# Kernel optimization log

Measured on AMD Instinct MI355X. Metric: run time of the kernel, lower is better.

The kernel has to match this reference:

```python
import jax, jax.numpy as jnp
import numpy as np

N = 100000      # nodes
E = 1250000     # edges
IN = 128        # in_channels
H = 64          # hidden_channels
L = 2           # num_layers (GCNConv count)
EPS = 1e-5      # BatchNorm eps


def setup_inputs() -> dict:
    key = jax.random.key(0)
    ks = jax.random.split(key, 10)
    x = jax.random.normal(ks[0], (N, IN), jnp.float32)
    edge_index = jax.random.randint(ks[1], (2, E), 0, N, dtype=jnp.int32)
    fc_w = jax.random.normal(ks[2], (IN, H), jnp.float32) / np.sqrt(IN)
    fc_b = jax.random.normal(ks[3], (H,), jnp.float32) * 0.01
    conv_w = jax.random.normal(ks[4], (L, H, H), jnp.float32) / np.sqrt(H)
    conv_b = jax.random.normal(ks[5], (L, H), jnp.float32) * 0.01
    bn_gamma = jnp.ones((L + 1, H), jnp.float32)
    bn_beta = jnp.zeros((L + 1, H), jnp.float32)
    bn_mean = jax.random.normal(ks[6], (L + 1, H), jnp.float32) * 0.1
    bn_var = jax.random.uniform(ks[7], (L + 1, H), jnp.float32) + 0.5
    return {"x": x, "edge_index": edge_index, "fc_w": fc_w, "fc_b": fc_b,
            "conv_w": conv_w, "conv_b": conv_b, "bn_gamma": bn_gamma,
            "bn_beta": bn_beta, "bn_mean": bn_mean, "bn_var": bn_var}


def reference(x, edge_index, fc_w, fc_b, conv_w, conv_b, bn_gamma, bn_beta, bn_mean, bn_var):
    n = x.shape[0]
    loops = jnp.arange(n, dtype=edge_index.dtype)
    src = jnp.concatenate([edge_index[0], loops])   # add self-loops (GCNConv default)
    dst = jnp.concatenate([edge_index[1], loops])
    # symmetric normalization: deg computed on destination, norm = d_s^-1/2 * d_d^-1/2
    deg = jax.ops.segment_sum(jnp.ones_like(dst, x.dtype), dst, num_segments=n)
    dis = jax.lax.rsqrt(deg)                        # deg >= 1 thanks to self-loops
    norm = dis[src] * dis[dst]                      # [E+N]

    def bn(h, i):  # eval-mode BatchNorm1d with running stats
        return (h - bn_mean[i]) * (bn_gamma[i] * jax.lax.rsqrt(bn_var[i] + EPS)) + bn_beta[i]

    h = jax.nn.relu(bn(x @ fc_w + fc_b, 0))         # [N, H]; dropout is identity in eval
    last = h
    for i in range(conv_w.shape[0]):
        hw = h @ conv_w[i]                          # GCNConv: transform then aggregate
        agg = jax.ops.segment_sum(hw[src] * norm[:, None], dst, num_segments=n) + conv_b[i]
        h = jax.nn.relu(bn(agg, i + 1)) + last      # residual to post-fc activation
    return h
```

## Files before the change

kernel.cpp:

```cpp
#include <hip/hip_runtime.h>

#define NNODES 100000
#define NEDGES 1250000
#define IN_CH 128
#define HID 64
#define BN_EPS 1e-5f

#define NPAD 100352
#define BIN_N 256
#define BINW 391
#define BIN_CHUNK 2048
#define BIN_BLOCKS 611
#define BIN_CAP_LDS 16
#define BIN_REGION 10000
#define MM_BLOCKS 1563
#define GBLOCKS 3125
#define ELL_C 32
#define OVF_CAP 65536

typedef __attribute__((ext_vector_type(8))) short s16x8;
typedef __attribute__((ext_vector_type(4))) float f32x4;

__device__ __forceinline__ ushort f2bf(float f) {
    union { float f; unsigned int i; } c;
    c.f = f;
    unsigned int lsb = (c.i >> 16) & 1u;
    return (ushort)((c.i + 0x7FFFu + lsb) >> 16);
}
__device__ __forceinline__ float asf(unsigned int i) {
    union { unsigned int i; float f; } c;
    c.i = i;
    return c.f;
}

__device__ __forceinline__ void ell_insert(int d, int soff, int* slot,
                                           int* ell, int* ovf_n, int2* ovf) {
    int s = atomicAdd(&slot[d], 1);
    if (s < ELL_C) ell[(d << 5) + s] = soff;
    else {
        int oi = atomicAdd(ovf_n, 1);
        if (oi < OVF_CAP) ovf[oi] = make_int2(d, soff);
    }
}

__device__ __forceinline__ void fc_body(
        int blk, int tid,
        const float* __restrict__ x, const float* __restrict__ w,
        const float* __restrict__ bb,
        const float* __restrict__ g, const float* __restrict__ be,
        const float* __restrict__ mu, const float* __restrict__ var,
        ushort* __restrict__ h0) {
    const int wave = tid >> 6;
    const int lane = tid & 63;
    const int m = lane & 15;
    const int q = lane >> 4;
    const int node_base = (blk * 4 + wave) * 16;

    s16x8 bfrag[4][4];
#pragma unroll
    for (int kc = 0; kc < 4; ++kc)
#pragma unroll
        for (int ct = 0; ct < 4; ++ct)
#pragma unroll
            for (int j = 0; j < 8; ++j)
                bfrag[kc][ct][j] = (short)f2bf(w[(kc * 32 + q * 8 + j) * HID + ct * 16 + m]);

    f32x4 acc[4] = {{0,0,0,0},{0,0,0,0},{0,0,0,0},{0,0,0,0}};

    int row = node_base + m;
    if (row >= NNODES) row = NNODES - 1;
    const float4* xp = (const float4*)(x + (size_t)row * IN_CH + q * 8);

#pragma unroll
    for (int kc = 0; kc < 4; ++kc) {
        float4 a0 = xp[kc * 8 + 0];
        float4 a1 = xp[kc * 8 + 1];
        s16x8 af;
        af[0] = (short)f2bf(a0.x); af[1] = (short)f2bf(a0.y);
        af[2] = (short)f2bf(a0.z); af[3] = (short)f2bf(a0.w);
        af[4] = (short)f2bf(a1.x); af[5] = (short)f2bf(a1.y);
        af[6] = (short)f2bf(a1.z); af[7] = (short)f2bf(a1.w);
#pragma unroll
        for (int ct = 0; ct < 4; ++ct)
            acc[ct] = __builtin_amdgcn_mfma_f32_16x16x32_bf16(af, bfrag[kc][ct], acc[ct], 0, 0, 0);
    }

#pragma unroll
    for (int ct = 0; ct < 4; ++ct) {
        int col = ct * 16 + m;
        float sc = g[col] * rsqrtf(var[col] + BN_EPS);
        float off = (bb[col] - mu[col]) * sc + be[col];
#pragma unroll
        for (int r = 0; r < 4; ++r) {
            int node = node_base + q * 4 + r;
            if (node < NNODES)
                h0[(size_t)node * HID + col] =
                    f2bf(fmaxf(acc[ct][r] * sc + off, 0.f));
        }
    }
}

__global__ __launch_bounds__(256) void bin_fc(
        const int* __restrict__ src, const int* __restrict__ dst,
        unsigned int* __restrict__ staged, int* bin_n,
        int* slot, int* __restrict__ ell, int* ovf_n, int2* __restrict__ ovf,
        const float* __restrict__ x, const float* __restrict__ w,
        const float* __restrict__ bb,
        const float* __restrict__ g, const float* __restrict__ be,
        const float* __restrict__ mu, const float* __restrict__ var,
        ushort* __restrict__ h0) {
    __shared__ unsigned int sbin[BIN_N][BIN_CAP_LDS];
    __shared__ int scnt[BIN_N];
    __shared__ int sbase[BIN_N];
    const int tid = threadIdx.x;

    if (blockIdx.x >= BIN_BLOCKS) {
        fc_body(blockIdx.x - BIN_BLOCKS, tid, x, w, bb, g, be, mu, var, h0);
        return;
    }

    scnt[tid] = 0;
    __syncthreads();

    const int base = blockIdx.x * (BIN_CHUNK / 4);
    const int4* dst4 = (const int4*)dst;
    const int4* src4 = (const int4*)src;
#pragma unroll
    for (int k = 0; k < BIN_CHUNK / 1024; ++k) {
        int i = base + k * 256 + tid;
        if (i < NEDGES / 4) {
            int4 dv = dst4[i];
            int4 sv = src4[i];
#define BIN_ONE(D, S)                                                       \
            {                                                               \
                int b_ = (D) / BINW;                                        \
                unsigned int pk_ = ((unsigned int)((D) - b_ * BINW) << 17)  \
                                   | (unsigned int)(S);                     \
                int sl_ = atomicAdd(&scnt[b_], 1);                          \
                if (sl_ < BIN_CAP_LDS) sbin[b_][sl_] = pk_;                 \
                else ell_insert((D), (S) << 7, slot, ell, ovf_n, ovf);      \
            }
            BIN_ONE(dv.x, sv.x)
            BIN_ONE(dv.y, sv.y)
            BIN_ONE(dv.z, sv.z)
            BIN_ONE(dv.w, sv.w)
#undef BIN_ONE
        }
    }
    __syncthreads();
    {
        int c = scnt[tid];
        if (c > BIN_CAP_LDS) c = BIN_CAP_LDS;
        sbase[tid] = atomicAdd(&bin_n[tid], c);
    }
    __syncthreads();
    const int wave = tid >> 6;
    const int lane = tid & 63;
    for (int grp = wave; grp < BIN_N / 4; grp += 4) {
        int b = grp * 4 + (lane >> 4);
        int s = lane & 15;
        int c = scnt[b];
        if (c > BIN_CAP_LDS) c = BIN_CAP_LDS;
        if (s < c) {
            int gidx = sbase[b] + s;
            unsigned int v = sbin[b][s];
            if (gidx < BIN_REGION) {
                staged[(size_t)b * BIN_REGION + gidx] = v;
            } else {
                int d = b * BINW + (int)(v >> 17);
                ell_insert(d, (int)(v & 0x1FFFFu) << 7, slot, ell, ovf_n, ovf);
            }
        }
    }
}

__global__ __launch_bounds__(1024) void ell_fill(
        const unsigned int* __restrict__ staged, const int* __restrict__ bin_n,
        int* slot, int* __restrict__ ell, int* ovf_n, int2* __restrict__ ovf) {
    const int b = blockIdx.x;
    int n = bin_n[b];
    if (n > BIN_REGION) n = BIN_REGION;
    const unsigned int* sp = staged + (size_t)b * BIN_REGION;
    const int lo = b * BINW;
    int i = threadIdx.x;
    for (; i + 3072 < n; i += 4096) {
        unsigned int v0 = sp[i];
        unsigned int v1 = sp[i + 1024];
        unsigned int v2 = sp[i + 2048];
        unsigned int v3 = sp[i + 3072];
        ell_insert(lo + (int)(v0 >> 17), (int)(v0 & 0x1FFFFu) << 7, slot, ell, ovf_n, ovf);
        ell_insert(lo + (int)(v1 >> 17), (int)(v1 & 0x1FFFFu) << 7, slot, ell, ovf_n, ovf);
        ell_insert(lo + (int)(v2 >> 17), (int)(v2 & 0x1FFFFu) << 7, slot, ell, ovf_n, ovf);
        ell_insert(lo + (int)(v3 >> 17), (int)(v3 & 0x1FFFFu) << 7, slot, ell, ovf_n, ovf);
    }
    for (; i < n; i += 1024) {
        unsigned int v = sp[i];
        ell_insert(lo + (int)(v >> 17), (int)(v & 0x1FFFFu) << 7, slot, ell, ovf_n, ovf);
    }
}

__global__ __launch_bounds__(256) void conv_mm_l1(
        const ushort* __restrict__ h, const float* __restrict__ w,
        const int* __restrict__ deg, ushort* __restrict__ hws) {
    const int tid = threadIdx.x;
    const int wave = tid >> 6;
    const int lane = tid & 63;
    const int m = lane & 15;
    const int q = lane >> 4;
    const int node_base = (blockIdx.x * 4 + wave) * 16;

    s16x8 bfrag[2][4];
#pragma unroll
    for (int kc = 0; kc < 2; ++kc)
#pragma unroll
        for (int ct = 0; ct < 4; ++ct)
#pragma unroll
            for (int j = 0; j < 8; ++j)
                bfrag[kc][ct][j] = (short)f2bf(w[(kc * 32 + q * 8 + j) * HID + ct * 16 + m]);

    f32x4 acc[4] = {{0,0,0,0},{0,0,0,0},{0,0,0,0},{0,0,0,0}};

    int row = node_base + m;
    if (row >= NNODES) row = NNODES - 1;

#pragma unroll
    for (int kc = 0; kc < 2; ++kc) {
        const s16x8* hp = (const s16x8*)(h + (size_t)row * HID + kc * 32 + q * 8);
        s16x8 af = *hp;
#pragma unroll
        for (int ct = 0; ct < 4; ++ct)
            acc[ct] = __builtin_amdgcn_mfma_f32_16x16x32_bf16(af, bfrag[kc][ct], acc[ct], 0, 0, 0);
    }

    float dv[4];
#pragma unroll
    for (int r = 0; r < 4; ++r) {
        int node = node_base + q * 4 + r;
        dv[r] = (node < NNODES) ? rsqrtf((float)(deg[node] + 1)) : 0.f;
    }
#pragma unroll
    for (int ct = 0; ct < 4; ++ct) {
#pragma unroll
        for (int r = 0; r < 4; ++r) {
            int node = node_base + q * 4 + r;
            if (node < NNODES)
                hws[(size_t)node * HID + ct * 16 + m] = f2bf(acc[ct][r] * dv[r]);
        }
    }
}

__global__ __launch_bounds__(256) void gather_conv(
        const ushort* __restrict__ hws,
        const int* __restrict__ deg, const int* __restrict__ ell,
        const int* __restrict__ ovf_n, const int2* __restrict__ ovf,
        const float* __restrict__ bias,
        const float* __restrict__ g, const float* __restrict__ be,
        const float* __restrict__ mu, const float* __restrict__ var,
        const ushort* __restrict__ last,
        const float* __restrict__ w2,
        ushort* __restrict__ hws2) {
    __shared__ ushort sh[32][72];
    const int wave = threadIdx.x >> 6;
    const int lane = threadIdx.x & 63;
    const int grp  = lane >> 3;
    const int j    = lane & 7;
    const int d = blockIdx.x * 32 + wave * 8 + grp;
    const unsigned int moff = (unsigned int)j * 16u;
    const unsigned int doff = ((unsigned int)d << 7) + moff;

    const char* hb = (const char*)hws;

    uint4 lv = *(const uint4*)((const char*)last + doff);

    float a[8];
    {
        uint4 sv = *(const uint4*)(hb + doff);
        a[0] = asf(sv.x << 16); a[1] = asf(sv.x & 0xffff0000u);
        a[2] = asf(sv.y << 16); a[3] = asf(sv.y & 0xffff0000u);
        a[4] = asf(sv.z << 16); a[5] = asf(sv.z & 0xffff0000u);
        a[6] = asf(sv.w << 16); a[7] = asf(sv.w & 0xffff0000u);
    }

#define ACC8(V)                                                         \
    a[0] += asf((V).x << 16); a[1] += asf((V).x & 0xffff0000u);         \
    a[2] += asf((V).y << 16); a[3] += asf((V).y & 0xffff0000u);         \
    a[4] += asf((V).z << 16); a[5] += asf((V).z & 0xffff0000u);         \
    a[6] += asf((V).w << 16); a[7] += asf((V).w & 0xffff0000u);

    const int n = deg[d];
    const int nn = (n < ELL_C) ? n : ELL_C;
    const int* sp = ell + ((size_t)d << 5);

    int k = 0;
    for (; k + 8 <= nn; k += 8) {
        unsigned int o0 = (unsigned int)sp[k + 0] + moff;
        unsigned int o1 = (unsigned int)sp[k + 1] + moff;
        unsigned int o2 = (unsigned int)sp[k + 2] + moff;
        unsigned int o3 = (unsigned int)sp[k + 3] + moff;
        unsigned int o4 = (unsigned int)sp[k + 4] + moff;
        unsigned int o5 = (unsigned int)sp[k + 5] + moff;
        unsigned int o6 = (unsigned int)sp[k + 6] + moff;
        unsigned int o7 = (unsigned int)sp[k + 7] + moff;
        uint4 v0 = *(const uint4*)(hb + o0);
        uint4 v1 = *(const uint4*)(hb + o1);
        uint4 v2 = *(const uint4*)(hb + o2);
        uint4 v3 = *(const uint4*)(hb + o3);
        uint4 v4 = *(const uint4*)(hb + o4);
        uint4 v5 = *(const uint4*)(hb + o5);
        uint4 v6 = *(const uint4*)(hb + o6);
        uint4 v7 = *(const uint4*)(hb + o7);
        ACC8(v0) ACC8(v1) ACC8(v2) ACC8(v3)
        ACC8(v4) ACC8(v5) ACC8(v6) ACC8(v7)
    }
    for (; k + 4 <= nn; k += 4) {
        unsigned int o0 = (unsigned int)sp[k + 0] + moff;
        unsigned int o1 = (unsigned int)sp[k + 1] + moff;
        unsigned int o2 = (unsigned int)sp[k + 2] + moff;
        unsigned int o3 = (unsigned int)sp[k + 3] + moff;
        uint4 v0 = *(const uint4*)(hb + o0);
        uint4 v1 = *(const uint4*)(hb + o1);
        uint4 v2 = *(const uint4*)(hb + o2);
        uint4 v3 = *(const uint4*)(hb + o3);
        ACC8(v0) ACC8(v1) ACC8(v2) ACC8(v3)
    }
    for (; k < nn; ++k) {
        uint4 v = *(const uint4*)(hb + ((unsigned int)sp[k] + moff));
        ACC8(v)
    }
    if (n > ELL_C) {
        int on = *ovf_n;
        if (on > OVF_CAP) on = OVF_CAP;
        for (int jj = 0; jj < on; ++jj) {
            int2 e = ovf[jj];
            if (e.x == d) {
                uint4 v = *(const uint4*)(hb + ((unsigned int)e.y + moff));
                ACC8(v)
            }
        }
    }
#undef ACC8

    float dd = rsqrtf((float)(n + 1));
    float4 bi0 = ((const float4*)bias)[2 * j], bi1 = ((const float4*)bias)[2 * j + 1];
    float4 g0  = ((const float4*)g)[2 * j],    g1  = ((const float4*)g)[2 * j + 1];
    float4 be0 = ((const float4*)be)[2 * j],   be1 = ((const float4*)be)[2 * j + 1];
    float4 mu0 = ((const float4*)mu)[2 * j],   mu1 = ((const float4*)mu)[2 * j + 1];
    float4 va0 = ((const float4*)var)[2 * j],  va1 = ((const float4*)var)[2 * j + 1];
    float l0 = asf(lv.x << 16), l1 = asf(lv.x & 0xffff0000u);
    float l2 = asf(lv.y << 16), l3 = asf(lv.y & 0xffff0000u);
    float l4 = asf(lv.z << 16), l5 = asf(lv.z & 0xffff0000u);
    float l6 = asf(lv.w << 16), l7 = asf(lv.w & 0xffff0000u);

#define EPI(A, BI, GV, BE, MU, VA, LO) \
    (fmaxf(((A) * dd + (BI) - (MU)) * ((GV) * rsqrtf((VA) + BN_EPS)) + (BE), 0.f) + (LO))
    float r0 = EPI(a[0], bi0.x, g0.x, be0.x, mu0.x, va0.x, l0);
    float r1 = EPI(a[1], bi0.y, g0.y, be0.y, mu0.y, va0.y, l1);
    float r2 = EPI(a[2], bi0.z, g0.z, be0.z, mu0.z, va0.z, l2);
    float r3 = EPI(a[3], bi0.w, g0.w, be0.w, mu0.w, va0.w, l3);
    float r4 = EPI(a[4], bi1.x, g1.x, be1.x, mu1.x, va1.x, l4);
    float r5 = EPI(a[5], bi1.y, g1.y, be1.y, mu1.y, va1.y, l5);
    float r6 = EPI(a[6], bi1.z, g1.z, be1.z, mu1.z, va1.z, l6);
    float r7 = EPI(a[7], bi1.w, g1.w, be1.w, mu1.w, va1.w, l7);
#undef EPI

    {
        const int rloc = wave * 8 + grp;
        uint4 o;
        o.x = (unsigned int)f2bf(r0 * dd) | ((unsigned int)f2bf(r1 * dd) << 16);
        o.y = (unsigned int)f2bf(r2 * dd) | ((unsigned int)f2bf(r3 * dd) << 16);
        o.z = (unsigned int)f2bf(r4 * dd) | ((unsigned int)f2bf(r5 * dd) << 16);
        o.w = (unsigned int)f2bf(r6 * dd) | ((unsigned int)f2bf(r7 * dd) << 16);
        *(uint4*)(&sh[rloc][j * 8]) = o;
    }
    __syncthreads();

    {
        const int rt = wave >> 1;
        const int cbase = (wave & 1) * 2;
        const int m = lane & 15;
        const int q = lane >> 4;

        s16x8 bfrag[2][2];
#pragma unroll
        for (int kc = 0; kc < 2; ++kc)
#pragma unroll
            for (int c = 0; c < 2; ++c)
#pragma unroll
                for (int jj = 0; jj < 8; ++jj)
                    bfrag[kc][c][jj] = (short)f2bf(
                        w2[(kc * 32 + q * 8 + jj) * HID + (cbase + c) * 16 + m]);

        f32x4 acc2[2] = {{0,0,0,0},{0,0,0,0}};
#pragma unroll
        for (int kc = 0; kc < 2; ++kc) {
            s16x8 af = *(const s16x8*)(&sh[rt * 16 + m][kc * 32 + q * 8]);
#pragma unroll
            for (int c = 0; c < 2; ++c)
                acc2[c] = __builtin_amdgcn_mfma_f32_16x16x32_bf16(
                    af, bfrag[kc][c], acc2[c], 0, 0, 0);
        }

        const int node_base = blockIdx.x * 32 + rt * 16;
#pragma unroll
        for (int c = 0; c < 2; ++c) {
            const int col = (cbase + c) * 16 + m;
#pragma unroll
            for (int r = 0; r < 4; ++r) {
                int node = node_base + q * 4 + r;
                hws2[(size_t)node * HID + col] = f2bf(acc2[c][r]);
            }
        }
    }
}

__global__ __launch_bounds__(256) void gather_update(
        const ushort* __restrict__ hws,
        const int* __restrict__ deg, const int* __restrict__ ell,
        const int* __restrict__ ovf_n, const int2* __restrict__ ovf,
        const float* __restrict__ bias,
        const float* __restrict__ g, const float* __restrict__ be,
        const float* __restrict__ mu, const float* __restrict__ var,
        const ushort* __restrict__ last,
        float* __restrict__ out_f) {
    const int wave = threadIdx.x >> 6;
    const int lane = threadIdx.x & 63;
    const int grp  = lane >> 3;
    const int j    = lane & 7;
    const int d = blockIdx.x * 32 + wave * 8 + grp;
    const unsigned int moff = (unsigned int)j * 16u;
    const unsigned int doff = ((unsigned int)d << 7) + moff;

    const char* hb = (const char*)hws;

    uint4 lv = *(const uint4*)((const char*)last + doff);

    float a[8];
    {
        uint4 sv = *(const uint4*)(hb + doff);
        a[0] = asf(sv.x << 16); a[1] = asf(sv.x & 0xffff0000u);
        a[2] = asf(sv.y << 16); a[3] = asf(sv.y & 0xffff0000u);
        a[4] = asf(sv.z << 16); a[5] = asf(sv.z & 0xffff0000u);
        a[6] = asf(sv.w << 16); a[7] = asf(sv.w & 0xffff0000u);
    }

#define ACC8(V)                                                         \
    a[0] += asf((V).x << 16); a[1] += asf((V).x & 0xffff0000u);         \
    a[2] += asf((V).y << 16); a[3] += asf((V).y & 0xffff0000u);         \
    a[4] += asf((V).z << 16); a[5] += asf((V).z & 0xffff0000u);         \
    a[6] += asf((V).w << 16); a[7] += asf((V).w & 0xffff0000u);

    const int n = deg[d];
    const int nn = (n < ELL_C) ? n : ELL_C;
    const int* sp = ell + ((size_t)d << 5);

    int k = 0;
    for (; k + 8 <= nn; k += 8) {
        unsigned int o0 = (unsigned int)sp[k + 0] + moff;
        unsigned int o1 = (unsigned int)sp[k + 1] + moff;
        unsigned int o2 = (unsigned int)sp[k + 2] + moff;
        unsigned int o3 = (unsigned int)sp[k + 3] + moff;
        unsigned int o4 = (unsigned int)sp[k + 4] + moff;
        unsigned int o5 = (unsigned int)sp[k + 5] + moff;
        unsigned int o6 = (unsigned int)sp[k + 6] + moff;
        unsigned int o7 = (unsigned int)sp[k + 7] + moff;
        uint4 v0 = *(const uint4*)(hb + o0);
        uint4 v1 = *(const uint4*)(hb + o1);
        uint4 v2 = *(const uint4*)(hb + o2);
        uint4 v3 = *(const uint4*)(hb + o3);
        uint4 v4 = *(const uint4*)(hb + o4);
        uint4 v5 = *(const uint4*)(hb + o5);
        uint4 v6 = *(const uint4*)(hb + o6);
        uint4 v7 = *(const uint4*)(hb + o7);
        ACC8(v0) ACC8(v1) ACC8(v2) ACC8(v3)
        ACC8(v4) ACC8(v5) ACC8(v6) ACC8(v7)
    }
    for (; k + 4 <= nn; k += 4) {
        unsigned int o0 = (unsigned int)sp[k + 0] + moff;
        unsigned int o1 = (unsigned int)sp[k + 1] + moff;
        unsigned int o2 = (unsigned int)sp[k + 2] + moff;
        unsigned int o3 = (unsigned int)sp[k + 3] + moff;
        uint4 v0 = *(const uint4*)(hb + o0);
        uint4 v1 = *(const uint4*)(hb + o1);
        uint4 v2 = *(const uint4*)(hb + o2);
        uint4 v3 = *(const uint4*)(hb + o3);
        ACC8(v0) ACC8(v1) ACC8(v2) ACC8(v3)
    }
    for (; k < nn; ++k) {
        uint4 v = *(const uint4*)(hb + ((unsigned int)sp[k] + moff));
        ACC8(v)
    }
    if (n > ELL_C) {
        int on = *ovf_n;
        if (on > OVF_CAP) on = OVF_CAP;
        for (int jj = 0; jj < on; ++jj) {
            int2 e = ovf[jj];
            if (e.x == d) {
                uint4 v = *(const uint4*)(hb + ((unsigned int)e.y + moff));
                ACC8(v)
            }
        }
    }
#undef ACC8

    float dd = rsqrtf((float)(n + 1));
    float4 bi0 = ((const float4*)bias)[2 * j], bi1 = ((const float4*)bias)[2 * j + 1];
    float4 g0  = ((const float4*)g)[2 * j],    g1  = ((const float4*)g)[2 * j + 1];
    float4 be0 = ((const float4*)be)[2 * j],   be1 = ((const float4*)be)[2 * j + 1];
    float4 mu0 = ((const float4*)mu)[2 * j],   mu1 = ((const float4*)mu)[2 * j + 1];
    float4 va0 = ((const float4*)var)[2 * j],  va1 = ((const float4*)var)[2 * j + 1];
    float l0 = asf(lv.x << 16), l1 = asf(lv.x & 0xffff0000u);
    float l2 = asf(lv.y << 16), l3 = asf(lv.y & 0xffff0000u);
    float l4 = asf(lv.z << 16), l5 = asf(lv.z & 0xffff0000u);
    float l6 = asf(lv.w << 16), l7 = asf(lv.w & 0xffff0000u);

#define EPI(A, BI, GV, BE, MU, VA, LO) \
    (fmaxf(((A) * dd + (BI) - (MU)) * ((GV) * rsqrtf((VA) + BN_EPS)) + (BE), 0.f) + (LO))
    float r0 = EPI(a[0], bi0.x, g0.x, be0.x, mu0.x, va0.x, l0);
    float r1 = EPI(a[1], bi0.y, g0.y, be0.y, mu0.y, va0.y, l1);
    float r2 = EPI(a[2], bi0.z, g0.z, be0.z, mu0.z, va0.z, l2);
    float r3 = EPI(a[3], bi0.w, g0.w, be0.w, mu0.w, va0.w, l3);
    float r4 = EPI(a[4], bi1.x, g1.x, be1.x, mu1.x, va1.x, l4);
    float r5 = EPI(a[5], bi1.y, g1.y, be1.y, mu1.y, va1.y, l5);
    float r6 = EPI(a[6], bi1.z, g1.z, be1.z, mu1.z, va1.z, l6);
    float r7 = EPI(a[7], bi1.w, g1.w, be1.w, mu1.w, va1.w, l7);
#undef EPI

    float4* op = (float4*)(out_f + (size_t)d * HID + j * 8);
    op[0] = make_float4(r0, r1, r2, r3);
    op[1] = make_float4(r4, r5, r6, r7);
}

extern "C" void kernel_launch(void* const* d_in, const int* in_sizes, int n_in,
                              void* d_out, int out_size, void* d_ws, size_t ws_size,
                              hipStream_t stream) {
    const float* x      = (const float*)d_in[0];
    const int*   eidx   = (const int*)d_in[1];
    const float* fc_w   = (const float*)d_in[2];
    const float* fc_b   = (const float*)d_in[3];
    const float* conv_w = (const float*)d_in[4];
    const float* conv_b = (const float*)d_in[5];
    const float* bn_g   = (const float*)d_in[6];
    const float* bn_b   = (const float*)d_in[7];
    const float* bn_m   = (const float*)d_in[8];
    const float* bn_v   = (const float*)d_in[9];

    const int* src = eidx;
    const int* dst = eidx + NEDGES;
    float* out = (float*)d_out;

    int*    slot    = (int*)d_ws;
    int*    meta    = slot + NPAD;
    int*    ovf_n   = meta;
    int*    bin_n   = meta + 16;
    int2*   ovf     = (int2*)(meta + 272);
    int*    ell     = (int*)(ovf + OVF_CAP);
    ushort* h0      = (ushort*)(ell + (size_t)NNODES * ELL_C);
    ushort* hws2    = h0 + (size_t)NNODES * HID;
    ushort* hws     = hws2 + (size_t)NNODES * HID;
    unsigned int* staged = (unsigned int*)(hws + (size_t)NNODES * HID);

    const int BLK = 256;

    hipMemsetAsync(slot, 0, (size_t)(NPAD + 272) * 4, stream);

    bin_fc<<<BIN_BLOCKS + MM_BLOCKS, BLK, 0, stream>>>(
        src, dst, staged, bin_n, slot, ell, ovf_n, ovf,
        x, fc_w, fc_b, bn_g, bn_b, bn_m, bn_v, h0);

    ell_fill<<<BIN_N, 1024, 0, stream>>>(staged, bin_n, slot, ell, ovf_n, ovf);

    conv_mm_l1<<<MM_BLOCKS, BLK, 0, stream>>>(h0, conv_w, slot, hws);

    gather_conv<<<GBLOCKS, BLK, 0, stream>>>(hws, slot, ell, ovf_n, ovf,
                                             conv_b, bn_g + HID, bn_b + HID,
                                             bn_m + HID, bn_v + HID, h0,
                                             conv_w + HID * HID, hws2);

    gather_update<<<GBLOCKS, BLK, 0, stream>>>(hws2, slot, ell, ovf_n, ovf,
                                               conv_b + HID, bn_g + 2 * HID, bn_b + 2 * HID,
                                               bn_m + 2 * HID, bn_v + 2 * HID,
                                               h0, out);
}
```

Measured before the change: 271.3 us.

## Fuse ELL fill with layer-1 matmul using block-local LDS slot counters

The ELL fill now runs per destination bin with slot counters kept in shared memory instead of global atomics, then writes the counts to global slot. The layer-1 transform matmul is fused into the same kernel, using the LDS degree counts for the normalisation, which removes one launch and the large slot memset. Edges that overflowed LDS during binning go to a first overflow list that every fill block scans, adding redundant reads in exchange for avoiding global atomics. The overflow capacity is reduced, and each bin's matmul over 391 nodes runs in two passes of 16-row tiles per wave.

```diff
diff --git a/kernel.cpp b/kernel.cpp
--- a/kernel.cpp
+++ b/kernel.cpp
@@ -16,7 +16,7 @@
 #define MM_BLOCKS 1563
 #define GBLOCKS 3125
 #define ELL_C 32
-#define OVF_CAP 65536
+#define OVF_CAP 16384
 
 typedef __attribute__((ext_vector_type(8))) short s16x8;
 typedef __attribute__((ext_vector_type(4))) float f32x4;
@@ -31,16 +31,6 @@
     union { unsigned int i; float f; } c;
     c.i = i;
     return c.f;
-}
-
-__device__ __forceinline__ void ell_insert(int d, int soff, int* slot,
-                                           int* ell, int* ovf_n, int2* ovf) {
-    int s = atomicAdd(&slot[d], 1);
-    if (s < ELL_C) ell[(d << 5) + s] = soff;
-    else {
-        int oi = atomicAdd(ovf_n, 1);
-        if (oi < OVF_CAP) ovf[oi] = make_int2(d, soff);
-    }
 }
 
 __device__ __forceinline__ void fc_body(
@@ -103,7 +93,7 @@
 __global__ __launch_bounds__(256) void bin_fc(
         const int* __restrict__ src, const int* __restrict__ dst,
         unsigned int* __restrict__ staged, int* bin_n,
-        int* slot, int* __restrict__ ell, int* ovf_n, int2* __restrict__ ovf,
+        int* ovf1_n, int2* __restrict__ ovf1,
         const float* __restrict__ x, const float* __restrict__ w,
         const float* __restrict__ bb,
         const float* __restrict__ g, const float* __restrict__ be,
@@ -138,7 +128,10 @@
                                    | (unsigned int)(S);                     \
                 int sl_ = atomicAdd(&scnt[b_], 1);                          \
                 if (sl_ < BIN_CAP_LDS) sbin[b_][sl_] = pk_;                 \
-                else ell_insert((D), (S) << 7, slot, ell, ovf_n, ovf);      \
+                else {                                                      \
+                    int oi_ = atomicAdd(ovf1_n, 1);                         \
+                    if (oi_ < OVF_CAP) ovf1[oi_] = make_int2((D), (S) << 7);\
+                }                                                           \
             }
             BIN_ONE(dv.x, sv.x)
             BIN_ONE(dv.y, sv.y)
@@ -168,46 +161,75 @@
                 staged[(size_t)b * BIN_REGION + gidx] = v;
             } else {
                 int d = b * BINW + (int)(v >> 17);
-                ell_insert(d, (int)(v & 0x1FFFFu) << 7, slot, ell, ovf_n, ovf);
+                int oi = atomicAdd(ovf1_n, 1);
+                if (oi < OVF_CAP) ovf1[oi] = make_int2(d, (int)(v & 0x1FFFFu) << 7);
             }
         }
     }
 }
 
-__global__ __launch_bounds__(1024) void ell_fill(
+__global__ __launch_bounds__(1024) void fill_conv(
         const unsigned int* __restrict__ staged, const int* __restrict__ bin_n,
-        int* slot, int* __restrict__ ell, int* ovf_n, int2* __restrict__ ovf) {
+        const int* __restrict__ ovf1_n, const int2* __restrict__ ovf1,
+        int* __restrict__ slot, int* __restrict__ ell,
+        int* ovf2_n, int2* __restrict__ ovf2,
+        const ushort* __restrict__ h0, const float* __restrict__ w1,
+        ushort* __restrict__ hws) {
+    __shared__ int cnt[BINW];
+    const int tid = threadIdx.x;
     const int b = blockIdx.x;
-    int n = bin_n[b];
-    if (n > BIN_REGION) n = BIN_REGION;
-    const unsigned int* sp = staged + (size_t)b * BIN_REGION;
     const int lo = b * BINW;
-    int i = threadIdx.x;
-    for (; i + 3072 < n; i += 4096) {
-        unsigned int v0 = sp[i];
-        unsigned int v1 = sp[i + 1024];
-        unsigned int v2 = sp[i + 2048];
-        unsigned int v3 = sp[i + 3072];
-        ell_insert(lo + (int)(v0 >> 17), (int)(v0 & 0x1FFFFu) << 7, slot, ell, ovf_n, ovf);
-        ell_insert(lo + (int)(v1 >> 17), (int)(v1 & 0x1FFFFu) << 7, slot, ell, ovf_n, ovf);
-        ell_insert(lo + (int)(v2 >> 17), (int)(v2 & 0x1FFFFu) << 7, slot, ell, ovf_n, ovf);
-        ell_insert(lo + (int)(v3 >> 17), (int)(v3 & 0x1FFFFu) << 7, slot, ell, ovf_n, ovf);
-    }
-    for (; i < n; i += 1024) {
-        unsigned int v = sp[i];
-        ell_insert(lo + (int)(v >> 17), (int)(v & 0x1FFFFu) << 7, slot, ell, ovf_n, ovf);
-    }
-}
-
-__global__ __launch_bounds__(256) void conv_mm_l1(
-        const ushort* __restrict__ h, const float* __restrict__ w,
-        const int* __restrict__ deg, ushort* __restrict__ hws) {
-    const int tid = threadIdx.x;
+    const int hi = (lo + BINW < NNODES) ? lo + BINW : NNODES;
+
+    for (int v = tid; v < BINW; v += 1024) cnt[v] = 0;
+    __syncthreads();
+
+#define INS(DL, SOFF)                                                       \
+    {                                                                       \
+        int s_ = atomicAdd(&cnt[(DL)], 1);                                  \
+        if (s_ < ELL_C) ell[((lo + (DL)) << 5) + s_] = (SOFF);              \
+        else {                                                              \
+            int oi_ = atomicAdd(ovf2_n, 1);                                 \
+            if (oi_ < OVF_CAP) ovf2[oi_] = make_int2(lo + (DL), (SOFF));    \
+        }                                                                   \
+    }
+    {
+        int n = bin_n[b];
+        if (n > BIN_REGION) n = BIN_REGION;
+        const unsigned int* sp = staged + (size_t)b * BIN_REGION;
+        int i = tid;
+        for (; i + 3072 < n; i += 4096) {
+            unsigned int v0 = sp[i];
+            unsigned int v1 = sp[i + 1024];
+            unsigned int v2 = sp[i + 2048];
+            unsigned int v3 = sp[i + 3072];
+            INS((int)(v0 >> 17), (int)(v0 & 0x1FFFFu) << 7)
+            INS((int)(v1 >> 17), (int)(v1 & 0x1FFFFu) << 7)
+            INS((int)(v2 >> 17), (int)(v2 & 0x1FFFFu) << 7)
+            INS((int)(v3 >> 17), (int)(v3 & 0x1FFFFu) << 7)
+        }
+        for (; i < n; i += 1024) {
+            unsigned int v = sp[i];
+            INS((int)(v >> 17), (int)(v & 0x1FFFFu) << 7)
+        }
+    }
+    {
+        int on = *ovf1_n;
+        if (on > OVF_CAP) on = OVF_CAP;
+        for (int i = tid; i < on; i += 1024) {
+            int2 e = ovf1[i];
+            if (e.x >= lo && e.x < hi) INS(e.x - lo, e.y)
+        }
+    }
+#undef INS
+    __syncthreads();
+
+    for (int v = tid; v < hi - lo; v += 1024) slot[lo + v] = cnt[v];
+
     const int wave = tid >> 6;
     const int lane = tid & 63;
     const int m = lane & 15;
     const int q = lane >> 4;
-    const int node_base = (blockIdx.x * 4 + wave) * 16;
 
     s16x8 bfrag[2][4];
 #pragma unroll
@@ -216,35 +238,39 @@
         for (int ct = 0; ct < 4; ++ct)
 #pragma unroll
             for (int j = 0; j < 8; ++j)
-                bfrag[kc][ct][j] = (short)f2bf(w[(kc * 32 + q * 8 + j) * HID + ct * 16 + m]);
-
-    f32x4 acc[4] = {{0,0,0,0},{0,0,0,0},{0,0,0,0},{0,0,0,0}};
-
-    int row = node_base + m;
-    if (row >= NNODES) row = NNODES - 1;
-
-#pragma unroll
-    for (int kc = 0; kc < 2; ++kc) {
-        const s16x8* hp = (const s16x8*)(h + (size_t)row * HID + kc * 32 + q * 8);
-        s16x8 af = *hp;
-#pragma unroll
-        for (int ct = 0; ct < 4; ++ct)
-            acc[ct] = __builtin_amdgcn_mfma_f32_16x16x32_bf16(af, bfrag[kc][ct], acc[ct], 0, 0, 0);
-    }
-
-    float dv[4];
-#pragma unroll
-    for (int r = 0; r < 4; ++r) {
-        int node = node_base + q * 4 + r;
-        dv[r] = (node < NNODES) ? rsqrtf((float)(deg[node] + 1)) : 0.f;
-    }
-#pragma unroll
-    for (int ct = 0; ct < 4; ++ct) {
+                bfrag[kc][ct][j] = (short)f2bf(w1[(kc * 32 + q * 8 + j) * HID + ct * 16 + m]);
+
+#pragma unroll
+    for (int pass = 0; pass < 2; ++pass) {
+        const int nb16 = lo + pass * 256 + wave * 16;
+        if (nb16 >= hi) continue;
+
+        f32x4 acc[4] = {{0,0,0,0},{0,0,0,0},{0,0,0,0},{0,0,0,0}};
+        int row = nb16 + m;
+        if (row >= hi) row = hi - 1;
+#pragma unroll
+        for (int kc = 0; kc < 2; ++kc) {
+            const s16x8* hp = (const s16x8*)(h0 + (size_t)row * HID + kc * 32 + q * 8);
+            s16x8 af = *hp;
+#pragma unroll
+            for (int ct = 0; ct < 4; ++ct)
+                acc[ct] = __builtin_amdgcn_mfma_f32_16x16x32_bf16(af, bfrag[kc][ct], acc[ct], 0, 0, 0);
+        }
+
+        float dv[4];
 #pragma unroll
         for (int r = 0; r < 4; ++r) {
-            int node = node_base + q * 4 + r;
-            if (node < NNODES)
-                hws[(size_t)node * HID + ct * 16 + m] = f2bf(acc[ct][r] * dv[r]);
+            int node = nb16 + q * 4 + r;
+            dv[r] = (node < hi) ? rsqrtf((float)(cnt[node - lo] + 1)) : 0.f;
+        }
+#pragma unroll
+        for (int ct = 0; ct < 4; ++ct) {
+#pragma unroll
+            for (int r = 0; r < 4; ++r) {
+                int node = nb16 + q * 4 + r;
+                if (node < hi)
+                    hws[(size_t)node * HID + ct * 16 + m] = f2bf(acc[ct][r] * dv[r]);
+            }
         }
     }
 }
@@ -550,10 +576,12 @@
 
     int*    slot    = (int*)d_ws;
     int*    meta    = slot + NPAD;
-    int*    ovf_n   = meta;
+    int*    ovf1_n  = meta;
+    int*    ovf2_n  = meta + 1;
     int*    bin_n   = meta + 16;
-    int2*   ovf     = (int2*)(meta + 272);
-    int*    ell     = (int*)(ovf + OVF_CAP);
+    int2*   ovf1    = (int2*)(meta + 272);
+    int2*   ovf2    = ovf1 + OVF_CAP;
+    int*    ell     = (int*)(ovf2 + OVF_CAP);
     ushort* h0      = (ushort*)(ell + (size_t)NNODES * ELL_C);
     ushort* hws2    = h0 + (size_t)NNODES * HID;
     ushort* hws     = hws2 + (size_t)NNODES * HID;
@@ -561,22 +589,22 @@
 
     const int BLK = 256;
 
-    hipMemsetAsync(slot, 0, (size_t)(NPAD + 272) * 4, stream);
+    hipMemsetAsync(meta, 0, 272 * 4, stream);
 
     bin_fc<<<BIN_BLOCKS + MM_BLOCKS, BLK, 0, stream>>>(
-        src, dst, staged, bin_n, slot, ell, ovf_n, ovf,
+        src, dst, staged, bin_n, ovf1_n, ovf1,
         x, fc_w, fc_b, bn_g, bn_b, bn_m, bn_v, h0);
 
-    ell_fill<<<BIN_N, 1024, 0, stream>>>(staged, bin_n, slot, ell, ovf_n, ovf);
-
-    conv_mm_l1<<<MM_BLOCKS, BLK, 0, stream>>>(h0, conv_w, slot, hws);
-
-    gather_conv<<<GBLOCKS, BLK, 0, stream>>>(hws, slot, ell, ovf_n, ovf,
+    fill_conv<<<BIN_N, 1024, 0, stream>>>(staged, bin_n, ovf1_n, ovf1,
+                                          slot, ell, ovf2_n, ovf2,
+                                          h0, conv_w, hws);
+
+    gather_conv<<<GBLOCKS, BLK, 0, stream>>>(hws, slot, ell, ovf2_n, ovf2,
                                              conv_b, bn_g + HID, bn_b + HID,
                                              bn_m + HID, bn_v + HID, h0,
                                              conv_w + HID * HID, hws2);
 
-    gather_update<<<GBLOCKS, BLK, 0, stream>>>(hws2, slot, ell, ovf_n, ovf,
+    gather_update<<<GBLOCKS, BLK, 0, stream>>>(hws2, slot, ell, ovf2_n, ovf2,
                                                conv_b + HID, bn_g + 2 * HID, bn_b + 2 * HID,
                                                bn_m + 2 * HID, bn_v + 2 * HID,
                                                h0, out);
```

After: 250.1 us. 1.08x faster.
